# Kernel optimization log

Measured on AMD Instinct MI355X. Metric: run time of the kernel, lower is better.

Reference implementation:

```python
import jax, jax.numpy as jnp
import numpy as np

NUM_NODES = 51681
EMBED_DIM = 32
HIDDEN_DIM = 64
NUM_EDGES = 2048  # input_dim == edge_weight.size(0)


def gcn_conv(x, W, b, src, dst, edge_weight, num_nodes):
    """PyG GCNConv with add_self_loops=True, symmetric normalization.
    x: [N, Fin], W: [Fin, Fout], b: [Fout], src/dst: [E], edge_weight: [E].
    """
    loop = jnp.arange(num_nodes)
    row = jnp.concatenate([src, loop])            # source of message
    col = jnp.concatenate([dst, loop])            # target (aggregation) node
    w = jnp.concatenate([edge_weight, jnp.ones((num_nodes,), x.dtype)])
    deg = jax.ops.segment_sum(w, col, num_segments=num_nodes)   # [N]
    dinv = jnp.where(deg > 0, jax.lax.rsqrt(deg), 0.0)
    norm = dinv[row] * w * dinv[col]              # [E+N]
    xw = x @ W                                    # [N, Fout]
    msgs = norm[:, None] * xw[row]                # gather + scale
    out = jax.ops.segment_sum(msgs, col, num_segments=num_nodes)
    return out + b


def setup_inputs() -> dict:
    key = jax.random.key(0)
    ks = jax.random.split(key, 12)
    edge_index = jax.random.randint(ks[0], (2, NUM_EDGES), 0, NUM_NODES)
    edge_weight = jax.random.uniform(ks[1], (NUM_EDGES,), dtype=jnp.float32)
    embedding = jax.random.normal(ks[2], (NUM_NODES, EMBED_DIM), jnp.float32)
    def lin(k, fin, fout):
        return jax.random.normal(k, (fin, fout), jnp.float32) / np.sqrt(fin)
    return {
        "edge_index": edge_index,
        "edge_weight": edge_weight,
        "embedding": embedding,
        "enc_W1": lin(ks[3], EMBED_DIM, HIDDEN_DIM),
        "enc_b1": jnp.zeros((HIDDEN_DIM,), jnp.float32),
        "enc_W2": lin(ks[4], HIDDEN_DIM, EMBED_DIM),
        "enc_b2": jnp.zeros((EMBED_DIM,), jnp.float32),
        "dec_W1": lin(ks[5], EMBED_DIM, HIDDEN_DIM),
        "dec_b1": jnp.zeros((HIDDEN_DIM,), jnp.float32),
        "dec_W2": lin(ks[6], HIDDEN_DIM, NUM_EDGES),
        "dec_b2": jnp.zeros((NUM_EDGES,), jnp.float32),
    }


def reference(edge_index, edge_weight, embedding,
              enc_W1, enc_b1, enc_W2, enc_b2,
              dec_W1, dec_b1, dec_W2, dec_b2):
    src, dst = edge_index[0], edge_index[1]
    # Encoder
    x = jax.nn.relu(gcn_conv(embedding, enc_W1, enc_b1, src, dst, edge_weight, NUM_NODES))
    z = jax.nn.relu(gcn_conv(x, enc_W2, enc_b2, src, dst, edge_weight, NUM_NODES))
    # Decoder
    h = jax.nn.relu(gcn_conv(z, dec_W1, dec_b1, src, dst, edge_weight, NUM_NODES))
    recon_x = gcn_conv(h, dec_W2, dec_b2, src, dst, edge_weight, NUM_NODES)
    return recon_x, z
```

## Files before the change

kernel.cpp:

```cpp
#include <hip/hip_runtime.h>

#define NN 51681
#define EE 2048
#define Z_OFF (51681LL * 2048LL)

typedef __bf16 bf16x8 __attribute__((ext_vector_type(8)));
typedef unsigned short ushort8 __attribute__((ext_vector_type(8)));
typedef float floatx4 __attribute__((ext_vector_type(4)));

__device__ inline unsigned short f2bf(float x) {
    unsigned u = __float_as_uint(x);
    unsigned r = (u + 0x7FFFu + ((u >> 16) & 1u)) >> 16;
    return (unsigned short)r;
}
__device__ inline float bf2f(unsigned short h) {
    return __uint_as_float(((unsigned)h) << 16);
}
__device__ inline void nt_store4(float* p, floatx4 v) {
    __builtin_nontemporal_store(v, reinterpret_cast<floatx4*>(p));
}


__global__ void init_k(const float* __restrict__ W4,
                       ushort* __restrict__ wthi, ushort* __restrict__ wtlo,
                       float* __restrict__ deg, const int* __restrict__ dst,
                       float* __restrict__ E4) {
    int b = blockIdx.x, t = threadIdx.x;
    if (b < 512) {
        int i = b * 256 + t;
        int k = i >> 11, c = i & 2047;
        float x = W4[i];
        ushort h = f2bf(x);
        ushort l = f2bf(x - bf2f(h));
        wthi[c * 64 + k] = h;
        wtlo[c * 64 + k] = l;
    } else if (b < 714) {
        int i = (b - 512) * 256 + t;
        if (i < NN) deg[i] = 1.0f;
    } else {
        int j = (b - 714) * 256 + t;
        int e = j >> 4, f = j & 15;
        reinterpret_cast<float4*>(&E4[(long long)dst[e] * 64])[f] =
            make_float4(0.f, 0.f, 0.f, 0.f);
    }
}

__global__ void deg_scatter_k(const int* __restrict__ dst, const float* __restrict__ w,
                              float* __restrict__ deg) {
    int e = blockIdx.x * 256 + threadIdx.x;
    if (e < EE) atomicAdd(&deg[dst[e]], w[e]);
}


__global__ void edge_scatter_k(const int* __restrict__ src, const int* __restrict__ dst,
                               const float* __restrict__ ew, const float* __restrict__ deg,
                               const float* __restrict__ X, float* __restrict__ E) {
    int tid = blockIdx.x * 256 + threadIdx.x;
    if (tid >= EE * 16) return;
    int e = tid >> 4;
    int f = (tid & 15) * 4;
    int s = src[e], d = dst[e];
    float n = rsqrtf(deg[s]) * ew[e] * rsqrtf(deg[d]);
    const float4 v = *reinterpret_cast<const float4*>(&X[(long long)s * 64 + f]);
    float* a = &E[(long long)d * 64 + f];
    atomicAdd(a + 0, n * v.x);
    atomicAdd(a + 1, n * v.y);
    atomicAdd(a + 2, n * v.z);
    atomicAdd(a + 3, n * v.w);
}


template<int K, int FOUT>
__global__ __launch_bounds__(256) void gemm_fused_k(
    const float* __restrict__ X,
    const int* __restrict__ src, const int* __restrict__ dst,
    const float* __restrict__ ew, const float* __restrict__ deg,
    const float* __restrict__ W, const float* __restrict__ bias,
    float* __restrict__ out) {
    constexpr int TPN = FOUT / 4;
    constexpr int NPB = 256 / TPN;
    __shared__ float Ws[K * FOUT];
    __shared__ float As[NPB][K + 4];
    __shared__ int qidx[EE];
    __shared__ int qcount;
    int tid = threadIdx.x;
    if (tid == 0) qcount = 0;
    for (int i = tid; i < K * FOUT / 4; i += 256)
        reinterpret_cast<float4*>(Ws)[i] = reinterpret_cast<const float4*>(W)[i];
    int node0 = blockIdx.x * NPB;
    for (int i = tid; i < NPB * (K / 4); i += 256) {
        int r = i / (K / 4);
        int kk = (i - r * (K / 4)) * 4;
        int g = node0 + r;
        float4 v = make_float4(0.f, 0.f, 0.f, 0.f);
        if (g < NN) {
            float s = 1.0f / deg[g];
            float4 xv = *reinterpret_cast<const float4*>(&X[(long long)g * K + kk]);
            v = make_float4(xv.x * s, xv.y * s, xv.z * s, xv.w * s);
        }
        *reinterpret_cast<float4*>(&As[r][kk]) = v;
    }
    __syncthreads();
    for (int e = tid; e < EE; e += 256) {
        unsigned r = (unsigned)(dst[e] - node0);
        if (r < (unsigned)NPB) { int s = atomicAdd(&qcount, 1); qidx[s] = e; }
    }
    __syncthreads();
    int nq = qcount;
    for (int qi = 0; qi < nq; ++qi) {
        int e = qidx[qi];
        int s_ = src[e], d_ = dst[e];
        float c = ew[e] * rsqrtf(deg[s_]) * rsqrtf(deg[d_]);
        int r = d_ - node0;
        if (tid < K) As[r][tid] += c * X[(long long)s_ * K + tid];
    }
    __syncthreads();
    int ln = tid / TPN;
    int n4 = (tid - ln * TPN) * 4;
    int g = node0 + ln;
    if (g >= NN) return;
    float4 acc = *reinterpret_cast<const float4*>(&bias[n4]);
    #pragma unroll
    for (int k = 0; k < K; ++k) {
        float a = As[ln][k];
        float4 w = *reinterpret_cast<const float4*>(&Ws[k * FOUT + n4]);
        acc.x = fmaf(a, w.x, acc.x);
        acc.y = fmaf(a, w.y, acc.y);
        acc.z = fmaf(a, w.z, acc.z);
        acc.w = fmaf(a, w.w, acc.w);
    }
    acc.x = fmaxf(acc.x, 0.f); acc.y = fmaxf(acc.y, 0.f);
    acc.z = fmaxf(acc.z, 0.f); acc.w = fmaxf(acc.w, 0.f);
    *reinterpret_cast<float4*>(&out[(long long)g * FOUT + n4]) = acc;
}


__global__ __launch_bounds__(512, 4) void gemm_big_k(
    const float* __restrict__ E, const float* __restrict__ H,
    const float* __restrict__ deg,
    const ushort* __restrict__ wthi, const ushort* __restrict__ wtlo,
    const float* __restrict__ bias, float* __restrict__ out) {
    __shared__ ushort Whi[128 * 64];
    __shared__ ushort Wlo[128 * 64];
    int tid  = threadIdx.x;
    int lane = tid & 63;
    int wv   = tid >> 6;
    int rl   = lane & 15;
    int kg   = lane >> 4;
    int cbase = blockIdx.x * 128;
    int node  = blockIdx.y * 128 + wv * 16 + rl;
    bool valid = node < NN;

    {
        const ushort8* sh8 = reinterpret_cast<const ushort8*>(wthi + (size_t)cbase * 64);
        const ushort8* sl8 = reinterpret_cast<const ushort8*>(wtlo + (size_t)cbase * 64);
        #pragma unroll
        for (int i = tid; i < 1024; i += 512) {
            int col = i >> 3, slot = i & 7;
            int d = col * 8 + (slot ^ (col & 7));
            reinterpret_cast<ushort8*>(Whi)[d] = sh8[i];
            reinterpret_cast<ushort8*>(Wlo)[d] = sl8[i];
        }
    }

    floatx4 bv[8];
    #pragma unroll
    for (int tl = 0; tl < 8; ++tl)
        bv[tl] = *reinterpret_cast<const floatx4*>(&bias[cbase + tl * 16 + kg * 4]);

    bf16x8 nb_hi[2], nb_lo[2];
    {
        float v[2][8];
        if (valid) {
            float dg = deg[node];
            float s = 1.0f / dg;
            const float* h0 = H + (long long)node * 64 + kg * 8;
            #pragma unroll
            for (int f = 0; f < 2; ++f) {
                float4 ha = *reinterpret_cast<const float4*>(h0 + f * 32);
                float4 hb = *reinterpret_cast<const float4*>(h0 + f * 32 + 4);
                v[f][0] = ha.x * s; v[f][1] = ha.y * s; v[f][2] = ha.z * s; v[f][3] = ha.w * s;
                v[f][4] = hb.x * s; v[f][5] = hb.y * s; v[f][6] = hb.z * s; v[f][7] = hb.w * s;
            }
            if (dg != 1.0f) {
                const float* e0 = E + (long long)node * 64 + kg * 8;
                #pragma unroll
                for (int f = 0; f < 2; ++f) {
                    float4 ea = *reinterpret_cast<const float4*>(e0 + f * 32);
                    float4 eb = *reinterpret_cast<const float4*>(e0 + f * 32 + 4);
                    v[f][0] += ea.x; v[f][1] += ea.y; v[f][2] += ea.z; v[f][3] += ea.w;
                    v[f][4] += eb.x; v[f][5] += eb.y; v[f][6] += eb.z; v[f][7] += eb.w;
                }
            }
        } else {
            #pragma unroll
            for (int f = 0; f < 2; ++f)
                #pragma unroll
                for (int i = 0; i < 8; ++i) v[f][i] = 0.f;
        }
        #pragma unroll
        for (int f = 0; f < 2; ++f) {
            ushort8 h8, l8;
            #pragma unroll
            for (int i = 0; i < 8; ++i) {
                unsigned u = __float_as_uint(v[f][i]) & 0xFFFF0000u;
                h8[i] = (unsigned short)(u >> 16);
                l8[i] = f2bf(v[f][i] - __uint_as_float(u));
            }
            nb_hi[f] = __builtin_bit_cast(bf16x8, h8);
            nb_lo[f] = __builtin_bit_cast(bf16x8, l8);
        }
    }

    __syncthreads();

    long long obase = (long long)node * 2048 + cbase + kg * 4;
    #pragma unroll
    for (int tl = 0; tl < 8; ++tl) {
        int col  = tl * 16 + rl;
        int base = col * 64;
        int s0 = (kg ^ (rl & 7)) * 8;
        int s1 = ((kg + 4) ^ (rl & 7)) * 8;
        bf16x8 wh0 = *reinterpret_cast<const bf16x8*>(&Whi[base + s0]);
        bf16x8 wh1 = *reinterpret_cast<const bf16x8*>(&Whi[base + s1]);
        bf16x8 wl0 = *reinterpret_cast<const bf16x8*>(&Wlo[base + s0]);
        bf16x8 wl1 = *reinterpret_cast<const bf16x8*>(&Wlo[base + s1]);

        floatx4 acc = bv[tl];
        acc = __builtin_amdgcn_mfma_f32_16x16x32_bf16(wh0, nb_hi[0], acc, 0, 0, 0);
        acc = __builtin_amdgcn_mfma_f32_16x16x32_bf16(wh0, nb_lo[0], acc, 0, 0, 0);
        acc = __builtin_amdgcn_mfma_f32_16x16x32_bf16(wl0, nb_hi[0], acc, 0, 0, 0);
        acc = __builtin_amdgcn_mfma_f32_16x16x32_bf16(wh1, nb_hi[1], acc, 0, 0, 0);
        acc = __builtin_amdgcn_mfma_f32_16x16x32_bf16(wh1, nb_lo[1], acc, 0, 0, 0);
        acc = __builtin_amdgcn_mfma_f32_16x16x32_bf16(wl1, nb_hi[1], acc, 0, 0, 0);

        if (valid)
            nt_store4(&out[obase + tl * 16], acc);
    }
}


extern "C" void kernel_launch(void* const* d_in, const int* in_sizes, int n_in,
                              void* d_out, int out_size, void* d_ws, size_t ws_size,
                              hipStream_t stream) {
    const int*   edge_index = (const int*)d_in[0];
    const int*   src = edge_index;
    const int*   dst = edge_index + EE;
    const float* ew  = (const float*)d_in[1];
    const float* emb = (const float*)d_in[2];
    const float* W1  = (const float*)d_in[3];
    const float* b1  = (const float*)d_in[4];
    const float* W2  = (const float*)d_in[5];
    const float* b2  = (const float*)d_in[6];
    const float* W3  = (const float*)d_in[7];
    const float* b3  = (const float*)d_in[8];
    const float* W4  = (const float*)d_in[9];
    const float* b4  = (const float*)d_in[10];

    float* out = (float*)d_out;
    float* z   = out + Z_OFF;

    float* ws   = (float*)d_ws;
    float* deg  = ws;
    float* E4   = ws + 51712;
    float* t1   = E4 + 3307584;
    ushort* wthi = (ushort*)(t1 + 3307584);
    ushort* wtlo = wthi + 131072;

    init_k<<<842, 256, 0, stream>>>(W4, wthi, wtlo, deg, dst, E4);
    deg_scatter_k<<<(EE + 255) / 256, 256, 0, stream>>>(dst, ew, deg);

    gemm_fused_k<32, 64><<<(NN + 15) / 16, 256, 0, stream>>>(
        emb, src, dst, ew, deg, W1, b1, t1);

    gemm_fused_k<64, 32><<<(NN + 31) / 32, 256, 0, stream>>>(
        t1, src, dst, ew, deg, W2, b2, z);

    gemm_fused_k<32, 64><<<(NN + 15) / 16, 256, 0, stream>>>(
        z, src, dst, ew, deg, W3, b3, t1);

    edge_scatter_k<<<(EE * 16 + 255) / 256, 256, 0, stream>>>(src, dst, ew, deg, t1, E4);
    gemm_big_k<<<dim3(16, 404), 512, 0, stream>>>(E4, t1, deg, wthi, wtlo, b4, out);
}
```

Baseline: 165.7 us.

## Drop W lo-split, widen column tile, stage outputs through LDS for coalesced stores

The final GEMM no longer splits the weights into bf16 hi/lo parts. It keeps only the bf16 high part and still splits the activations, which cuts the MFMA count per tile from 6 to 4 and lowers precision on the weight side. Each block now covers 256 output columns instead of 128, halving the grid in x and holding 16 accumulators per lane. Results are transposed through shared memory in four rounds so each row of 1 KB is written contiguously with non-temporal stores, replacing the earlier strided 16-byte stores. The trade-off is more register pressure, with launch bounds occupancy lowered to 2, plus extra barriers.

```diff
diff --git a/kernel.cpp b/kernel.cpp
--- a/kernel.cpp
+++ b/kernel.cpp
@@ -13,27 +13,20 @@
     unsigned r = (u + 0x7FFFu + ((u >> 16) & 1u)) >> 16;
     return (unsigned short)r;
 }
-__device__ inline float bf2f(unsigned short h) {
-    return __uint_as_float(((unsigned)h) << 16);
-}
 __device__ inline void nt_store4(float* p, floatx4 v) {
     __builtin_nontemporal_store(v, reinterpret_cast<floatx4*>(p));
 }
 
 
 __global__ void init_k(const float* __restrict__ W4,
-                       ushort* __restrict__ wthi, ushort* __restrict__ wtlo,
+                       ushort* __restrict__ wthi,
                        float* __restrict__ deg, const int* __restrict__ dst,
                        float* __restrict__ E4) {
     int b = blockIdx.x, t = threadIdx.x;
     if (b < 512) {
         int i = b * 256 + t;
         int k = i >> 11, c = i & 2047;
-        float x = W4[i];
-        ushort h = f2bf(x);
-        ushort l = f2bf(x - bf2f(h));
-        wthi[c * 64 + k] = h;
-        wtlo[c * 64 + k] = l;
+        wthi[c * 64 + k] = f2bf(W4[i]);
     } else if (b < 714) {
         int i = (b - 512) * 256 + t;
         if (i < NN) deg[i] = 1.0f;
@@ -135,38 +128,35 @@
 }
 
 
-__global__ __launch_bounds__(512, 4) void gemm_big_k(
+__global__ __launch_bounds__(512, 2) void gemm_big_k(
     const float* __restrict__ E, const float* __restrict__ H,
     const float* __restrict__ deg,
-    const ushort* __restrict__ wthi, const ushort* __restrict__ wtlo,
+    const ushort* __restrict__ wthi,
     const float* __restrict__ bias, float* __restrict__ out) {
-    __shared__ ushort Whi[128 * 64];
-    __shared__ ushort Wlo[128 * 64];
+    __shared__ ushort Whi[256 * 64];
     int tid  = threadIdx.x;
     int lane = tid & 63;
     int wv   = tid >> 6;
     int rl   = lane & 15;
     int kg   = lane >> 4;
-    int cbase = blockIdx.x * 128;
+    int cbase = blockIdx.x * 256;
     int node  = blockIdx.y * 128 + wv * 16 + rl;
     bool valid = node < NN;
 
     {
         const ushort8* sh8 = reinterpret_cast<const ushort8*>(wthi + (size_t)cbase * 64);
-        const ushort8* sl8 = reinterpret_cast<const ushort8*>(wtlo + (size_t)cbase * 64);
         #pragma unroll
-        for (int i = tid; i < 1024; i += 512) {
+        for (int i = tid; i < 2048; i += 512) {
             int col = i >> 3, slot = i & 7;
             int d = col * 8 + (slot ^ (col & 7));
             reinterpret_cast<ushort8*>(Whi)[d] = sh8[i];
-            reinterpret_cast<ushort8*>(Wlo)[d] = sl8[i];
-        }
-    }
-
-    floatx4 bv[8];
-    #pragma unroll
-    for (int tl = 0; tl < 8; ++tl)
-        bv[tl] = *reinterpret_cast<const floatx4*>(&bias[cbase + tl * 16 + kg * 4]);
+        }
+    }
+
+    floatx4 acc[16];
+    #pragma unroll
+    for (int tl = 0; tl < 16; ++tl)
+        acc[tl] = *reinterpret_cast<const floatx4*>(&bias[cbase + tl * 16 + kg * 4]);
 
     bf16x8 nb_hi[2], nb_lo[2];
     {
@@ -214,28 +204,44 @@
 
     __syncthreads();
 
-    long long obase = (long long)node * 2048 + cbase + kg * 4;
-    #pragma unroll
-    for (int tl = 0; tl < 8; ++tl) {
+    #pragma unroll
+    for (int tl = 0; tl < 16; ++tl) {
         int col  = tl * 16 + rl;
         int base = col * 64;
         int s0 = (kg ^ (rl & 7)) * 8;
         int s1 = ((kg + 4) ^ (rl & 7)) * 8;
         bf16x8 wh0 = *reinterpret_cast<const bf16x8*>(&Whi[base + s0]);
         bf16x8 wh1 = *reinterpret_cast<const bf16x8*>(&Whi[base + s1]);
-        bf16x8 wl0 = *reinterpret_cast<const bf16x8*>(&Wlo[base + s0]);
-        bf16x8 wl1 = *reinterpret_cast<const bf16x8*>(&Wlo[base + s1]);
-
-        floatx4 acc = bv[tl];
-        acc = __builtin_amdgcn_mfma_f32_16x16x32_bf16(wh0, nb_hi[0], acc, 0, 0, 0);
-        acc = __builtin_amdgcn_mfma_f32_16x16x32_bf16(wh0, nb_lo[0], acc, 0, 0, 0);
-        acc = __builtin_amdgcn_mfma_f32_16x16x32_bf16(wl0, nb_hi[0], acc, 0, 0, 0);
-        acc = __builtin_amdgcn_mfma_f32_16x16x32_bf16(wh1, nb_hi[1], acc, 0, 0, 0);
-        acc = __builtin_amdgcn_mfma_f32_16x16x32_bf16(wh1, nb_lo[1], acc, 0, 0, 0);
-        acc = __builtin_amdgcn_mfma_f32_16x16x32_bf16(wl1, nb_hi[1], acc, 0, 0, 0);
-
-        if (valid)
-            nt_store4(&out[obase + tl * 16], acc);
+        acc[tl] = __builtin_amdgcn_mfma_f32_16x16x32_bf16(wh0, nb_hi[0], acc[tl], 0, 0, 0);
+        acc[tl] = __builtin_amdgcn_mfma_f32_16x16x32_bf16(wh0, nb_lo[0], acc[tl], 0, 0, 0);
+        acc[tl] = __builtin_amdgcn_mfma_f32_16x16x32_bf16(wh1, nb_hi[1], acc[tl], 0, 0, 0);
+        acc[tl] = __builtin_amdgcn_mfma_f32_16x16x32_bf16(wh1, nb_lo[1], acc[tl], 0, 0, 0);
+    }
+
+    __syncthreads();
+
+    float* stg = reinterpret_cast<float*>(Whi);
+    int rowbase = blockIdx.y * 128 + wv * 16;
+    int sseg = lane >> 2, sj = lane & 3;
+    #pragma unroll
+    for (int round = 0; round < 4; ++round) {
+        if ((wv >> 1) == round) {
+            float* patch = stg + (wv & 1) * 4096;
+            #pragma unroll
+            for (int tl = 0; tl < 16; ++tl) {
+                int w = rl * 256 + ((tl ^ rl) & 15) * 16 + kg * 4;
+                *reinterpret_cast<floatx4*>(&patch[w]) = acc[tl];
+            }
+            #pragma unroll
+            for (int r = 0; r < 16; ++r) {
+                int w = r * 256 + ((sseg ^ r) & 15) * 16 + sj * 4;
+                floatx4 v = *reinterpret_cast<const floatx4*>(&patch[w]);
+                int gr = rowbase + r;
+                if (gr < NN)
+                    nt_store4(&out[(long long)gr * 2048 + cbase + lane * 4], v);
+            }
+        }
+        __syncthreads();
     }
 }
 
@@ -265,9 +271,8 @@
     float* E4   = ws + 51712;
     float* t1   = E4 + 3307584;
     ushort* wthi = (ushort*)(t1 + 3307584);
-    ushort* wtlo = wthi + 131072;
-
-    init_k<<<842, 256, 0, stream>>>(W4, wthi, wtlo, deg, dst, E4);
+
+    init_k<<<842, 256, 0, stream>>>(W4, wthi, deg, dst, E4);
     deg_scatter_k<<<(EE + 255) / 256, 256, 0, stream>>>(dst, ew, deg);
 
     gemm_fused_k<32, 64><<<(NN + 15) / 16, 256, 0, stream>>>(
@@ -280,5 +285,5 @@
         z, src, dst, ew, deg, W3, b3, t1);
 
     edge_scatter_k<<<(EE * 16 + 255) / 256, 256, 0, stream>>>(src, dst, ew, deg, t1, E4);
-    gemm_big_k<<<dim3(16, 404), 512, 0, stream>>>(E4, t1, deg, wthi, wtlo, b4, out);
-}
+    gemm_big_k<<<dim3(8, 404), 512, 0, stream>>>(E4, t1, deg, wthi, b4, out);
+}
```

Result: faster. 152.6 us (-7.9%).
